# Performance work log

Hardware: AMD Instinct MI355X
Metric: run time of the kernel (lower is better)

## Reference

```python
import jax, jax.numpy as jnp
import numpy as np

GAMMA = 0.999   # from TDLoss.__init__ default
LAMBDA = 0.95   # from compute_gae default lambda_
B, S = 8192, 2048


def setup_inputs() -> dict:
    key = jax.random.key(0)
    k1, k2, k3, k4 = jax.random.split(key, 4)
    rewards = jax.random.normal(k1, (B, S), dtype=jnp.float32)
    values = jax.random.normal(k2, (B, S), dtype=jnp.float32)
    dones = jax.random.randint(k3, (B, S), 0, 2).astype(jnp.int32)
    # prefix validity mask: valid_len[b] = mask[b].sum(), as assumed by compute_gae
    lengths = jax.random.randint(k4, (B,), S // 2, S + 1)
    mask = (jnp.arange(S)[None, :] < lengths[:, None]).astype(jnp.int32)
    return {"rewards": rewards, "values": values, "dones": dones, "mask": mask}


def _gae(rewards, values, dones_f, mask, gamma, lam):
    # rewards/values/dones_f: [B,S] float; mask: [B,S] int prefix mask
    b, s = rewards.shape
    valid_len = mask.sum(axis=1)                      # [B]
    t_idx = jnp.arange(s)
    valid = t_idx[None, :] < valid_len[:, None]       # [B,S] bool
    is_last = t_idx[None, :] == (valid_len[:, None] - 1)
    # next_value = values[:, t+1], except 0 at the last valid step (and at t=S-1)
    next_vals = jnp.concatenate([values[:, 1:], jnp.zeros((b, 1), values.dtype)], axis=1)
    next_vals = jnp.where(is_last, jnp.zeros((), values.dtype), next_vals)
    nd = 1.0 - dones_f                                # (1 - done)
    delta = rewards + gamma * next_vals * nd - values

    def step(gae, xs):
        d_t, nd_t, valid_t = xs                        # each [B]
        g = d_t + gamma * lam * nd_t * gae
        g = jnp.where(valid_t, g, jnp.zeros((), d_t.dtype))  # zero outside valid prefix; resets carry
        return g, g

    xs = (delta.T, nd.T, valid.T)                     # time-major [S,B]
    _, adv_t = jax.lax.scan(step, jnp.zeros(b, rewards.dtype), xs, reverse=True)
    advantages = adv_t.T                              # [B,S]
    returns = jnp.where(valid, advantages + values, jnp.zeros((), values.dtype))
    return advantages, returns


def reference(rewards, values, dones, mask):
    return _gae(rewards, values, dones.astype(jnp.float32), mask, GAMMA, LAMBDA)
```

## Files before the change

kernel.cpp:

```cpp
#include <hip/hip_runtime.h>


static constexpr int BATCH = 8192;
static constexpr int SEQ   = 2048;
static constexpr int EPL   = 8;
static constexpr float GAMMA  = 0.999f;
static constexpr float LAMBDA = 0.95f;
static constexpr float GL     = GAMMA * LAMBDA;

__global__ __launch_bounds__(256, 4) void gae_kernel(
    const float* __restrict__ rewards,
    const float* __restrict__ values,
    const int*   __restrict__ dones,
    const int*   __restrict__ mask,
    float*       __restrict__ out)
{
    __shared__ float sA[4], sB[4], sF[4];

    const int lane = threadIdx.x & 63;
    const int wave = threadIdx.x >> 6;
    const int row  = blockIdx.x;
    const size_t off = (size_t)row * SEQ + (size_t)threadIdx.x * EPL;

    float rr[EPL], vv[EPL];
    int   dd[EPL], mm[EPL];
    {
        const float4 r0 = *reinterpret_cast<const float4*>(rewards + off);
        const float4 r1 = *reinterpret_cast<const float4*>(rewards + off + 4);
        const float4 v0 = *reinterpret_cast<const float4*>(values  + off);
        const float4 v1 = *reinterpret_cast<const float4*>(values  + off + 4);
        const int4   d0 = *reinterpret_cast<const int4*>(dones + off);
        const int4   d1 = *reinterpret_cast<const int4*>(dones + off + 4);
        const int4   m0 = *reinterpret_cast<const int4*>(mask  + off);
        const int4   m1 = *reinterpret_cast<const int4*>(mask  + off + 4);
        rr[0]=r0.x; rr[1]=r0.y; rr[2]=r0.z; rr[3]=r0.w;
        rr[4]=r1.x; rr[5]=r1.y; rr[6]=r1.z; rr[7]=r1.w;
        vv[0]=v0.x; vv[1]=v0.y; vv[2]=v0.z; vv[3]=v0.w;
        vv[4]=v1.x; vv[5]=v1.y; vv[6]=v1.z; vv[7]=v1.w;
        dd[0]=d0.x; dd[1]=d0.y; dd[2]=d0.z; dd[3]=d0.w;
        dd[4]=d1.x; dd[5]=d1.y; dd[6]=d1.z; dd[7]=d1.w;
        mm[0]=m0.x; mm[1]=m0.y; mm[2]=m0.z; mm[3]=m0.w;
        mm[4]=m1.x; mm[5]=m1.y; mm[6]=m1.z; mm[7]=m1.w;
    }

    float a[EPL], b[EPL], vm[EPL], mr[EPL], mnd[EPL];
    #pragma unroll
    for (int e = 0; e < EPL; ++e) {
        const bool m  = (mm[e] != 0);
        const bool mn = m && (dd[e] == 0);
        vm[e]  = m ? vv[e] : 0.0f;
        mr[e]  = m ? rr[e] : 0.0f;
        mnd[e] = mn ? 1.0f : 0.0f;
        a[e]   = mn ? GL : 0.0f;
    }

    if (lane == 0) sF[wave] = vm[0];
    __syncthreads();

    float nv7 = __shfl_down(vm[0], 1, 64);
    if (lane == 63) nv7 = (wave < 3) ? sF[wave + 1] : 0.0f;

    #pragma unroll
    for (int e = 0; e < EPL; ++e) {
        const float nv = (e < EPL - 1) ? vm[e + 1] : nv7;
        b[e] = mr[e] + GAMMA * nv * mnd[e] - vm[e];
    }

    float A = a[EPL - 1], B = b[EPL - 1];
    #pragma unroll
    for (int e = EPL - 2; e >= 0; --e) {
        B = fmaf(a[e], B, b[e]);
        A = a[e] * A;
    }

    float As = A, Bs = B;
    #pragma unroll
    for (int d = 1; d < 64; d <<= 1) {
        const float Ao = __shfl_down(As, d, 64);
        const float Bo = __shfl_down(Bs, d, 64);
        if (lane + d < 64) {
            Bs = fmaf(As, Bo, Bs);
            As = As * Ao;
        }
    }

    if (lane == 0) { sA[wave] = As; sB[wave] = Bs; }
    __syncthreads();
    float C = 0.0f;
    for (int w2 = 3; w2 > wave; --w2)
        C = fmaf(sA[w2], C, sB[w2]);

    float cA = __shfl_down(As, 1, 64);
    float cB = __shfl_down(Bs, 1, 64);
    if (lane == 63) { cA = 1.0f; cB = 0.0f; }
    float g = fmaf(cA, C, cB);

    float adv[EPL], ret[EPL];
    #pragma unroll
    for (int e = EPL - 1; e >= 0; --e) {
        g = fmaf(a[e], g, b[e]);
        adv[e] = g;
        ret[e] = g + vm[e];
    }

    float* ap = out + off;
    float* tp = out + (size_t)BATCH * SEQ + off;
    *reinterpret_cast<float4*>(ap)     = make_float4(adv[0], adv[1], adv[2], adv[3]);
    *reinterpret_cast<float4*>(ap + 4) = make_float4(adv[4], adv[5], adv[6], adv[7]);
    *reinterpret_cast<float4*>(tp)     = make_float4(ret[0], ret[1], ret[2], ret[3]);
    *reinterpret_cast<float4*>(tp + 4) = make_float4(ret[4], ret[5], ret[6], ret[7]);
}

extern "C" void kernel_launch(void* const* d_in, const int* in_sizes, int n_in,
                              void* d_out, int out_size, void* d_ws, size_t ws_size,
                              hipStream_t stream) {
    const float* rewards = (const float*)d_in[0];
    const float* values  = (const float*)d_in[1];
    const int*   dones   = (const int*)d_in[2];
    const int*   mask    = (const int*)d_in[3];
    float* out = (float*)d_out;

    dim3 grid(BATCH), block(256);
    gae_kernel<<<grid, block, 0, stream>>>(rewards, values, dones, mask, out);
}
```

Measured before the change: 322.7 us.

## Process four rows per block with software-prefetched next-row loads and nontemporal stores

Each block now handles four rows in sequence and issues the global loads for the next row before the current row's scan and stores. This is meant to hide load latency behind the intra-block scan and cut per-block launch and sync overhead. Output writes become nontemporal stores to reduce cache pollution. The cost is higher register pressure from keeping a second row's raw data live, and fewer blocks in the grid.

```diff
diff --git a/kernel.cpp b/kernel.cpp
--- a/kernel.cpp
+++ b/kernel.cpp
@@ -4,9 +4,35 @@
 static constexpr int BATCH = 8192;
 static constexpr int SEQ   = 2048;
 static constexpr int EPL   = 8;
+static constexpr int ROWS  = 4;
 static constexpr float GAMMA  = 0.999f;
 static constexpr float LAMBDA = 0.95f;
 static constexpr float GL     = GAMMA * LAMBDA;
+
+typedef float fx4 __attribute__((ext_vector_type(4)));
+typedef int   ix4 __attribute__((ext_vector_type(4)));
+
+struct Raw {
+    fx4 r0, r1, v0, v1;
+    ix4 d0, d1, m0, m1;
+};
+
+__device__ __forceinline__ Raw load_row(const float* __restrict__ R,
+                                        const float* __restrict__ V,
+                                        const int*   __restrict__ D,
+                                        const int*   __restrict__ M,
+                                        size_t off) {
+    Raw x;
+    x.r0 = *reinterpret_cast<const fx4*>(R + off);
+    x.r1 = *reinterpret_cast<const fx4*>(R + off + 4);
+    x.v0 = *reinterpret_cast<const fx4*>(V + off);
+    x.v1 = *reinterpret_cast<const fx4*>(V + off + 4);
+    x.d0 = *reinterpret_cast<const ix4*>(D + off);
+    x.d1 = *reinterpret_cast<const ix4*>(D + off + 4);
+    x.m0 = *reinterpret_cast<const ix4*>(M + off);
+    x.m1 = *reinterpret_cast<const ix4*>(M + off + 4);
+    return x;
+}
 
 __global__ __launch_bounds__(256, 4) void gae_kernel(
     const float* __restrict__ rewards,
@@ -15,100 +41,105 @@
     const int*   __restrict__ mask,
     float*       __restrict__ out)
 {
-    __shared__ float sA[4], sB[4], sF[4];
+    __shared__ float sF[2][4], sA[2][4], sB[2][4];
 
     const int lane = threadIdx.x & 63;
     const int wave = threadIdx.x >> 6;
-    const int row  = blockIdx.x;
-    const size_t off = (size_t)row * SEQ + (size_t)threadIdx.x * EPL;
+    const int row0 = blockIdx.x * ROWS;
+    const size_t tof = (size_t)threadIdx.x * EPL;
 
-    float rr[EPL], vv[EPL];
-    int   dd[EPL], mm[EPL];
-    {
-        const float4 r0 = *reinterpret_cast<const float4*>(rewards + off);
-        const float4 r1 = *reinterpret_cast<const float4*>(rewards + off + 4);
-        const float4 v0 = *reinterpret_cast<const float4*>(values  + off);
-        const float4 v1 = *reinterpret_cast<const float4*>(values  + off + 4);
-        const int4   d0 = *reinterpret_cast<const int4*>(dones + off);
-        const int4   d1 = *reinterpret_cast<const int4*>(dones + off + 4);
-        const int4   m0 = *reinterpret_cast<const int4*>(mask  + off);
-        const int4   m1 = *reinterpret_cast<const int4*>(mask  + off + 4);
-        rr[0]=r0.x; rr[1]=r0.y; rr[2]=r0.z; rr[3]=r0.w;
-        rr[4]=r1.x; rr[5]=r1.y; rr[6]=r1.z; rr[7]=r1.w;
-        vv[0]=v0.x; vv[1]=v0.y; vv[2]=v0.z; vv[3]=v0.w;
-        vv[4]=v1.x; vv[5]=v1.y; vv[6]=v1.z; vv[7]=v1.w;
-        dd[0]=d0.x; dd[1]=d0.y; dd[2]=d0.z; dd[3]=d0.w;
-        dd[4]=d1.x; dd[5]=d1.y; dd[6]=d1.z; dd[7]=d1.w;
-        mm[0]=m0.x; mm[1]=m0.y; mm[2]=m0.z; mm[3]=m0.w;
-        mm[4]=m1.x; mm[5]=m1.y; mm[6]=m1.z; mm[7]=m1.w;
-    }
-
-    float a[EPL], b[EPL], vm[EPL], mr[EPL], mnd[EPL];
-    #pragma unroll
-    for (int e = 0; e < EPL; ++e) {
-        const bool m  = (mm[e] != 0);
-        const bool mn = m && (dd[e] == 0);
-        vm[e]  = m ? vv[e] : 0.0f;
-        mr[e]  = m ? rr[e] : 0.0f;
-        mnd[e] = mn ? 1.0f : 0.0f;
-        a[e]   = mn ? GL : 0.0f;
-    }
-
-    if (lane == 0) sF[wave] = vm[0];
-    __syncthreads();
-
-    float nv7 = __shfl_down(vm[0], 1, 64);
-    if (lane == 63) nv7 = (wave < 3) ? sF[wave + 1] : 0.0f;
+    Raw cur = load_row(rewards, values, dones, mask, (size_t)row0 * SEQ + tof);
 
     #pragma unroll
-    for (int e = 0; e < EPL; ++e) {
-        const float nv = (e < EPL - 1) ? vm[e + 1] : nv7;
-        b[e] = mr[e] + GAMMA * nv * mnd[e] - vm[e];
+    for (int r = 0; r < ROWS; ++r) {
+        const int p = r & 1;
+        const size_t off = (size_t)(row0 + r) * SEQ + tof;
+
+        const float rr[EPL] = {cur.r0.x, cur.r0.y, cur.r0.z, cur.r0.w,
+                               cur.r1.x, cur.r1.y, cur.r1.z, cur.r1.w};
+        const float vv[EPL] = {cur.v0.x, cur.v0.y, cur.v0.z, cur.v0.w,
+                               cur.v1.x, cur.v1.y, cur.v1.z, cur.v1.w};
+        const int   dd[EPL] = {cur.d0.x, cur.d0.y, cur.d0.z, cur.d0.w,
+                               cur.d1.x, cur.d1.y, cur.d1.z, cur.d1.w};
+        const int   mm[EPL] = {cur.m0.x, cur.m0.y, cur.m0.z, cur.m0.w,
+                               cur.m1.x, cur.m1.y, cur.m1.z, cur.m1.w};
+
+        float a[EPL], b[EPL], vm[EPL];
+        #pragma unroll
+        for (int e = 0; e < EPL; ++e) {
+            const bool m  = (mm[e] != 0);
+            const bool mn = m && (dd[e] == 0);
+            vm[e] = m ? vv[e] : 0.0f;
+            a[e]  = mn ? GL : 0.0f;
+        }
+
+        if (lane == 0) sF[p][wave] = vm[0];
+        __syncthreads();
+        float nv7 = __shfl_down(vm[0], 1, 64);
+        if (lane == 63) nv7 = (wave < 3) ? sF[p][wave + 1] : 0.0f;
+
+        #pragma unroll
+        for (int e = 0; e < EPL; ++e) {
+            const bool  m   = (mm[e] != 0);
+            const bool  mn  = m && (dd[e] == 0);
+            const float mr  = m ? rr[e] : 0.0f;
+            const float mnd = mn ? 1.0f : 0.0f;
+            const float nv  = (e < EPL - 1) ? vm[e + 1] : nv7;
+            b[e] = mr + GAMMA * nv * mnd - vm[e];
+        }
+
+        Raw nxt;
+        if (r + 1 < ROWS)
+            nxt = load_row(rewards, values, dones, mask, off + SEQ);
+
+        float A = a[EPL - 1], B = b[EPL - 1];
+        #pragma unroll
+        for (int e = EPL - 2; e >= 0; --e) {
+            B = fmaf(a[e], B, b[e]);
+            A = a[e] * A;
+        }
+
+        float As = A, Bs = B;
+        #pragma unroll
+        for (int d = 1; d < 64; d <<= 1) {
+            const float Ao = __shfl_down(As, d, 64);
+            const float Bo = __shfl_down(Bs, d, 64);
+            if (lane + d < 64) {
+                Bs = fmaf(As, Bo, Bs);
+                As = As * Ao;
+            }
+        }
+
+        if (lane == 0) { sA[p][wave] = As; sB[p][wave] = Bs; }
+        __syncthreads();
+        float C = 0.0f;
+        for (int w2 = 3; w2 > wave; --w2)
+            C = fmaf(sA[p][w2], C, sB[p][w2]);
+
+        float cA = __shfl_down(As, 1, 64);
+        float cB = __shfl_down(Bs, 1, 64);
+        if (lane == 63) { cA = 1.0f; cB = 0.0f; }
+        float g = fmaf(cA, C, cB);
+
+        float adv[EPL], ret[EPL];
+        #pragma unroll
+        for (int e = EPL - 1; e >= 0; --e) {
+            g = fmaf(a[e], g, b[e]);
+            adv[e] = g;
+            ret[e] = g + vm[e];
+        }
+
+        fx4 a0 = {adv[0], adv[1], adv[2], adv[3]};
+        fx4 a1 = {adv[4], adv[5], adv[6], adv[7]};
+        fx4 t0 = {ret[0], ret[1], ret[2], ret[3]};
+        fx4 t1 = {ret[4], ret[5], ret[6], ret[7]};
+        __builtin_nontemporal_store(a0, reinterpret_cast<fx4*>(out + off));
+        __builtin_nontemporal_store(a1, reinterpret_cast<fx4*>(out + off + 4));
+        __builtin_nontemporal_store(t0, reinterpret_cast<fx4*>(out + (size_t)BATCH * SEQ + off));
+        __builtin_nontemporal_store(t1, reinterpret_cast<fx4*>(out + (size_t)BATCH * SEQ + off + 4));
+
+        if (r + 1 < ROWS) cur = nxt;
     }
-
-    float A = a[EPL - 1], B = b[EPL - 1];
-    #pragma unroll
-    for (int e = EPL - 2; e >= 0; --e) {
-        B = fmaf(a[e], B, b[e]);
-        A = a[e] * A;
-    }
-
-    float As = A, Bs = B;
-    #pragma unroll
-    for (int d = 1; d < 64; d <<= 1) {
-        const float Ao = __shfl_down(As, d, 64);
-        const float Bo = __shfl_down(Bs, d, 64);
-        if (lane + d < 64) {
-            Bs = fmaf(As, Bo, Bs);
-            As = As * Ao;
-        }
-    }
-
-    if (lane == 0) { sA[wave] = As; sB[wave] = Bs; }
-    __syncthreads();
-    float C = 0.0f;
-    for (int w2 = 3; w2 > wave; --w2)
-        C = fmaf(sA[w2], C, sB[w2]);
-
-    float cA = __shfl_down(As, 1, 64);
-    float cB = __shfl_down(Bs, 1, 64);
-    if (lane == 63) { cA = 1.0f; cB = 0.0f; }
-    float g = fmaf(cA, C, cB);
-
-    float adv[EPL], ret[EPL];
-    #pragma unroll
-    for (int e = EPL - 1; e >= 0; --e) {
-        g = fmaf(a[e], g, b[e]);
-        adv[e] = g;
-        ret[e] = g + vm[e];
-    }
-
-    float* ap = out + off;
-    float* tp = out + (size_t)BATCH * SEQ + off;
-    *reinterpret_cast<float4*>(ap)     = make_float4(adv[0], adv[1], adv[2], adv[3]);
-    *reinterpret_cast<float4*>(ap + 4) = make_float4(adv[4], adv[5], adv[6], adv[7]);
-    *reinterpret_cast<float4*>(tp)     = make_float4(ret[0], ret[1], ret[2], ret[3]);
-    *reinterpret_cast<float4*>(tp + 4) = make_float4(ret[4], ret[5], ret[6], ret[7]);
 }
 
 extern "C" void kernel_launch(void* const* d_in, const int* in_sizes, int n_in,
@@ -120,6 +151,6 @@
     const int*   mask    = (const int*)d_in[3];
     float* out = (float*)d_out;
 
-    dim3 grid(BATCH), block(256);
+    dim3 grid(BATCH / ROWS), block(256);
     gae_kernel<<<grid, block, 0, stream>>>(rewards, values, dones, mask, out);
 }
```

Result: slower. 334.9 us (+3.8%).
